# Optimization experiments

Measured on AMD Instinct MI355X. Metric: run time of the kernel, lower is better.

## Reference

```python
import jax, jax.numpy as jnp
import numpy as np

N_NODES = 100000
N_EDGES = 3200000
EMB = 64
K = 2
NUM_GRAPHS = 512


def setup_inputs() -> dict:
    key = jax.random.key(0)
    ks = jax.random.split(key, 12)
    x = jax.random.normal(ks[0], (N_NODES, EMB), dtype=jnp.float32)
    edge_index = jax.random.randint(ks[1], (2, N_EDGES), 0, N_NODES, dtype=jnp.int64)
    edge_attr = jax.random.normal(ks[2], (N_EDGES, 1), dtype=jnp.float32)
    batch = jnp.sort(jax.random.randint(ks[3], (N_NODES,), 0, NUM_GRAPHS, dtype=jnp.int64))
    s = 1.0 / np.sqrt(EMB)
    wn1 = jax.random.normal(ks[4], (EMB, EMB), dtype=jnp.float32) * s
    bn1 = jnp.zeros((EMB,), jnp.float32)
    wn2 = jax.random.normal(ks[5], (EMB, 1), dtype=jnp.float32) * s
    bn2 = jnp.zeros((1,), jnp.float32)
    wc1 = jax.random.normal(ks[6], (EMB, EMB), dtype=jnp.float32) * s
    bc1 = jnp.zeros((EMB,), jnp.float32)
    wc2 = jax.random.normal(ks[7], (EMB, 2 * K * EMB), dtype=jnp.float32) * s
    bc2 = jnp.zeros((2 * K * EMB,), jnp.float32)
    return dict(x=x, edge_index=edge_index, edge_attr=edge_attr, batch=batch,
                wn1=wn1, bn1=bn1, wn2=wn2, bn2=bn2,
                wc1=wc1, bc1=bc1, wc2=wc2, bc2=bc2)


def reference(x, edge_index, edge_attr, batch, wn1, bn1, wn2, bn2, wc1, bc1, wc2, bc2):
    N, C = x.shape
    alpha = 0.1  # APPNP teleport prob
    # --- APPNP(K=1): gcn_norm with self-loops, one propagation step ---
    loops = jnp.arange(N, dtype=edge_index.dtype)
    src = jnp.concatenate([edge_index[0], loops])
    dst = jnp.concatenate([edge_index[1], loops])
    ones = jnp.ones(src.shape[0], dtype=x.dtype)
    deg = jax.ops.segment_sum(ones, dst, num_segments=N)
    dinv = jnp.where(deg > 0, jax.lax.rsqrt(deg), 0.0)
    norm = dinv[src] * dinv[dst]  # [E+N]
    agg = jax.ops.segment_sum(x[src] * norm[:, None], dst, num_segments=N)
    diffuse_x = (1.0 - alpha) * agg + alpha * x  # [N, C]
    # --- node-wise gate: MLP -> global softmax over all nodes ---
    h = jax.nn.relu(diffuse_x @ wn1 + bn1)
    gamma = h @ wn2 + bn2  # [N, 1]
    gamma = jax.nn.softmax(gamma, axis=0)
    # --- per-graph mean pool + channel-wise MLP ---
    sums = jax.ops.segment_sum(diffuse_x, batch, num_segments=NUM_GRAPHS)
    cnt = jax.ops.segment_sum(jnp.ones((N,), x.dtype), batch, num_segments=NUM_GRAPHS)
    pooled = jnp.where(cnt[:, None] > 0, sums / jnp.maximum(cnt, 1.0)[:, None], 0.0)
    pc = jnp.tanh(jax.nn.relu(pooled @ wc1 + bc1) @ wc2 + bc2)  # [B, 2*K*C]
    alpha_kc = pc[:, : K * C].reshape(NUM_GRAPHS, K, C)
    beta_kc = alpha_kc  # faithful to original bug: beta_kc = alpha_kc.reshape(...)
    # --- per-node affine via kron(alpha_kc, gamma_dense) gathered back to nodes ---
    # alpha_batch[b, n, k, c] = alpha_kc[b, k, c] * gamma_dense[b, n]; mask-gather == index by batch
    g = gamma[:, :, None]  # [N, 1, 1]
    a_node = alpha_kc[batch] * g  # [N, K, C]
    b_node = beta_kc[batch] * g  # [N, K, C]
    out = jnp.max(a_node * x[:, None, :] + b_node, axis=1)  # [N, C]
    return out
```

## Files before the change

### kernel.cpp

```cpp
#include <hip/hip_runtime.h>
#include <cstdint>

#define N_NODES   100000
#define N_EDGES   3200000
#define EMB       64
#define NUM_GRAPHS 512
#define NB        391
#define CAP       9216
#define PCHUNK    8192
#define PBLOCKS   391

__device__ __forceinline__ float bflo(unsigned u) { return __uint_as_float(u << 16); }
__device__ __forceinline__ float bfhi(unsigned u) { return __uint_as_float(u & 0xFFFF0000u); }
__device__ __forceinline__ unsigned rne_bf16(float f) {
    unsigned b = __float_as_uint(f);
    return (b + 0x7FFFu + ((b >> 16) & 1u)) >> 16;
}

__global__ void cvt_kernel(const float* __restrict__ x, unsigned* __restrict__ xh) {
    int i = blockIdx.x * 256 + threadIdx.x;
    if (i < N_NODES * EMB / 2) {
        float2 f = ((const float2*)x)[i];
        xh[i] = rne_bf16(f.x) | (rne_bf16(f.y) << 16);
    }
}

__global__ void partition_kernel(const int* __restrict__ ei, int* __restrict__ bcnt,
                                 unsigned* __restrict__ gpairs) {
    __shared__ unsigned sp[PCHUNK];
    __shared__ int scnt[512];
    __shared__ int soff[512];
    __shared__ int scur[512];
    __shared__ int gbase[512];
    __shared__ int s[256];
    int t = threadIdx.x;
    for (int i = t; i < 512; i += 256) scnt[i] = 0;
    __syncthreads();
    int base = blockIdx.x * PCHUNK;
    int lim  = min(N_EDGES - base, PCHUNK);
    for (int k = t; k < lim; k += 256) {
        int d = ei[N_EDGES + base + k];
        atomicAdd(&scnt[d >> 8], 1);
    }
    __syncthreads();
    int a0 = scnt[2 * t], a1 = scnt[2 * t + 1];
    int p = a0 + a1;
    s[t] = p; __syncthreads();
    for (int d = 1; d < 256; d <<= 1) {
        int add = (t >= d) ? s[t - d] : 0;
        __syncthreads();
        s[t] += add;
        __syncthreads();
    }
    int excl = s[t] - p;
    soff[2 * t] = excl;       soff[2 * t + 1] = excl + a0;
    scur[2 * t] = excl;       scur[2 * t + 1] = excl + a0;
    __syncthreads();
    for (int i = t; i < NB; i += 256) gbase[i] = i * CAP + atomicAdd(&bcnt[i], scnt[i]);
    __syncthreads();
    for (int k = t; k < lim; k += 256) {
        int sId = ei[base + k];
        int d   = ei[N_EDGES + base + k];
        int pos = atomicAdd(&scur[d >> 8], 1);
        sp[pos] = (unsigned)sId | ((unsigned)(d & 255) << 17);
    }
    __syncthreads();
    for (int i = t; i < lim; i += 256) {
        unsigned pk = sp[i];
        int lo = 0, hi = NB - 1;
        while (lo < hi) { int mid = (lo + hi + 1) >> 1; if (soff[mid] <= i) lo = mid; else hi = mid - 1; }
        gpairs[gbase[lo] + (i - soff[lo])] = pk;
    }
}

__global__ void bucket_scan_kernel(const int* __restrict__ bcnt, int* __restrict__ bbase) {
    __shared__ int s[512];
    int t = threadIdx.x;
    int v = (t < NB) ? bcnt[t] : 0;
    s[t] = v; __syncthreads();
    for (int d = 1; d < 512; d <<= 1) {
        int add = (t >= d) ? s[t - d] : 0;
        __syncthreads();
        s[t] += add;
        __syncthreads();
    }
    if (t < NB) bbase[t] = s[t] - v;
}

__global__ void bscatter2_kernel(const unsigned* __restrict__ gpairs, const int* __restrict__ bcnt,
                                 const int* __restrict__ bbase, int* __restrict__ ebuf,
                                 int* __restrict__ indeg, int* __restrict__ rowstart,
                                 float* __restrict__ dinv) {
    int b = blockIdx.x, t = threadIdx.x, nlo = b << 8;
    __shared__ int lcnt[256];
    __shared__ int lcur[256];
    __shared__ int s[256];
    lcnt[t] = 0; __syncthreads();
    int cnt = bcnt[b];
    const unsigned* gp = gpairs + (size_t)b * CAP;
    for (int i = t; i < cnt; i += 256) atomicAdd(&lcnt[(gp[i] >> 17) & 255], 1);
    __syncthreads();
    int v = lcnt[t];
    s[t] = v; __syncthreads();
    for (int d = 1; d < 256; d <<= 1) {
        int add = (t >= d) ? s[t - d] : 0;
        __syncthreads();
        s[t] += add;
        __syncthreads();
    }
    int excl = s[t] - v;
    int base = bbase[b];
    int n = nlo + t;
    if (n < N_NODES) {
        indeg[n] = v;
        rowstart[n] = base + excl;
        dinv[n] = rsqrtf((float)(v + 1));
    }
    lcur[t] = base + excl;
    __syncthreads();
    for (int i = t; i < cnt; i += 256) {
        unsigned pk = gp[i];
        int pos = atomicAdd(&lcur[(pk >> 17) & 255], 1);
        ebuf[pos] = (int)(pk & 0x1FFFFu);
    }
}

__global__ void gather_mlp_bf16(const int* __restrict__ ebuf, const int* __restrict__ rowstart,
                                const int* __restrict__ indeg, const float* __restrict__ dinv,
                                const float* __restrict__ x, const unsigned* __restrict__ xh,
                                float* __restrict__ dx,
                                const float* __restrict__ wn1, const float* __restrict__ bn1,
                                const float* __restrict__ wn2, const float* __restrict__ bn2,
                                float* __restrict__ gl) {
    __shared__ float wn1s[EMB * EMB];
    __shared__ float bn1s[EMB];
    __shared__ float wn2s[EMB];
    for (int i = threadIdx.x; i < EMB * EMB; i += blockDim.x) wn1s[i] = wn1[i];
    if (threadIdx.x < EMB) { bn1s[threadIdx.x] = bn1[threadIdx.x]; wn2s[threadIdx.x] = wn2[threadIdx.x]; }
    __syncthreads();

    int wid = (blockIdx.x * blockDim.x + threadIdx.x) >> 6;
    if (wid >= N_NODES) return;
    int n = __builtin_amdgcn_readfirstlane(wid);
    int l = threadIdx.x & 63;
    int g = l >> 3;
    int q = l & 7;
    int start = rowstart[n];
    int cnt   = indeg[n];
    float dn  = dinv[n];
    const uint4* __restrict__ xr = (const uint4*)xh;

    float a0 = 0.f, a1 = 0.f, a2 = 0.f, a3 = 0.f, a4 = 0.f, a5 = 0.f, a6 = 0.f, a7 = 0.f;
    int j = 0;
    for (; j + 16 <= cnt; j += 16) {
        int sA = ebuf[start + j + g];
        int sB = ebuf[start + j + 8 + g];
        float wA = dinv[sA] * dn;
        float wB = dinv[sB] * dn;
        uint4 vA = xr[sA * 8 + q];
        uint4 vB = xr[sB * 8 + q];
        a0 += bflo(vA.x) * wA + bflo(vB.x) * wB;
        a1 += bfhi(vA.x) * wA + bfhi(vB.x) * wB;
        a2 += bflo(vA.y) * wA + bflo(vB.y) * wB;
        a3 += bfhi(vA.y) * wA + bfhi(vB.y) * wB;
        a4 += bflo(vA.z) * wA + bflo(vB.z) * wB;
        a5 += bfhi(vA.z) * wA + bfhi(vB.z) * wB;
        a6 += bflo(vA.w) * wA + bflo(vB.w) * wB;
        a7 += bfhi(vA.w) * wA + bfhi(vB.w) * wB;
    }
    if (j + 8 <= cnt) {
        int sA = ebuf[start + j + g];
        float wA = dinv[sA] * dn;
        uint4 vA = xr[sA * 8 + q];
        a0 += bflo(vA.x) * wA; a1 += bfhi(vA.x) * wA;
        a2 += bflo(vA.y) * wA; a3 += bfhi(vA.y) * wA;
        a4 += bflo(vA.z) * wA; a5 += bfhi(vA.z) * wA;
        a6 += bflo(vA.w) * wA; a7 += bfhi(vA.w) * wA;
        j += 8;
    }
    if (g < cnt - j) {
        int sA = ebuf[start + j + g];
        float wA = dinv[sA] * dn;
        uint4 vA = xr[sA * 8 + q];
        a0 += bflo(vA.x) * wA; a1 += bfhi(vA.x) * wA;
        a2 += bflo(vA.y) * wA; a3 += bfhi(vA.y) * wA;
        a4 += bflo(vA.z) * wA; a5 += bfhi(vA.z) * wA;
        a6 += bflo(vA.w) * wA; a7 += bfhi(vA.w) * wA;
    }
    a0 += __shfl_xor(a0, 8); a0 += __shfl_xor(a0, 16); a0 += __shfl_xor(a0, 32);
    a1 += __shfl_xor(a1, 8); a1 += __shfl_xor(a1, 16); a1 += __shfl_xor(a1, 32);
    a2 += __shfl_xor(a2, 8); a2 += __shfl_xor(a2, 16); a2 += __shfl_xor(a2, 32);
    a3 += __shfl_xor(a3, 8); a3 += __shfl_xor(a3, 16); a3 += __shfl_xor(a3, 32);
    a4 += __shfl_xor(a4, 8); a4 += __shfl_xor(a4, 16); a4 += __shfl_xor(a4, 32);
    a5 += __shfl_xor(a5, 8); a5 += __shfl_xor(a5, 16); a5 += __shfl_xor(a5, 32);
    a6 += __shfl_xor(a6, 8); a6 += __shfl_xor(a6, 16); a6 += __shfl_xor(a6, 32);
    a7 += __shfl_xor(a7, 8); a7 += __shfl_xor(a7, 16); a7 += __shfl_xor(a7, 32);

    const float4* __restrict__ x4 = (const float4*)x;
    float4 xv0 = x4[n * 16 + 2 * q];
    float4 xv1 = x4[n * 16 + 2 * q + 1];
    float s2 = dn * dn;
    float r0 = 0.9f * (a0 + xv0.x * s2) + 0.1f * xv0.x;
    float r1 = 0.9f * (a1 + xv0.y * s2) + 0.1f * xv0.y;
    float r2 = 0.9f * (a2 + xv0.z * s2) + 0.1f * xv0.z;
    float r3 = 0.9f * (a3 + xv0.w * s2) + 0.1f * xv0.w;
    float r4 = 0.9f * (a4 + xv1.x * s2) + 0.1f * xv1.x;
    float r5 = 0.9f * (a5 + xv1.y * s2) + 0.1f * xv1.y;
    float r6 = 0.9f * (a6 + xv1.z * s2) + 0.1f * xv1.z;
    float r7 = 0.9f * (a7 + xv1.w * s2) + 0.1f * xv1.w;
    if (l < 8) {
        float4 w0; w0.x = r0; w0.y = r1; w0.z = r2; w0.w = r3;
        float4 w1; w1.x = r4; w1.y = r5; w1.z = r6; w1.w = r7;
        ((float4*)dx)[n * 16 + 2 * l]     = w0;
        ((float4*)dx)[n * 16 + 2 * l + 1] = w1;
    }

    float rr[8] = {r0, r1, r2, r3, r4, r5, r6, r7};
    float am = bn1s[l];
#pragma unroll
    for (int c = 0; c < EMB; ++c) {
        float b = __shfl(rr[c & 7], c >> 3);
        am += b * wn1s[c * EMB + l];
    }
    float h = fmaxf(am, 0.0f);
    float t = h * wn2s[l];
#pragma unroll
    for (int off = 32; off; off >>= 1) t += __shfl_xor(t, off);
    if (l == 0) gl[n] = t + bn2[0];
}

__global__ void gather_mlp_kernel(const int* __restrict__ ebuf, const int* __restrict__ rowstart,
                                  const int* __restrict__ indeg, const float* __restrict__ dinv,
                                  const float* __restrict__ x, float* __restrict__ dx,
                                  const float* __restrict__ wn1, const float* __restrict__ bn1,
                                  const float* __restrict__ wn2, const float* __restrict__ bn2,
                                  float* __restrict__ gl) {
    __shared__ float wn1s[EMB * EMB];
    __shared__ float bn1s[EMB];
    __shared__ float wn2s[EMB];
    for (int i = threadIdx.x; i < EMB * EMB; i += blockDim.x) wn1s[i] = wn1[i];
    if (threadIdx.x < EMB) { bn1s[threadIdx.x] = bn1[threadIdx.x]; wn2s[threadIdx.x] = wn2[threadIdx.x]; }
    __syncthreads();

    int wid = (blockIdx.x * blockDim.x + threadIdx.x) >> 6;
    if (wid >= N_NODES) return;
    int n = __builtin_amdgcn_readfirstlane(wid);
    int l = threadIdx.x & 63;
    int g = l >> 4;
    int q = l & 15;
    int start = rowstart[n];
    int cnt   = indeg[n];
    float dn  = dinv[n];
    const float4* __restrict__ x4 = (const float4*)x;

    float ax = 0.f, ay = 0.f, az = 0.f, aw = 0.f;
    int j = 0;
    for (; j + 8 <= cnt; j += 8) {
        int sA = ebuf[start + j + g];
        int sB = ebuf[start + j + 4 + g];
        float wA = dinv[sA] * dn;
        float wB = dinv[sB] * dn;
        float4 vA = x4[sA * 16 + q];
        float4 vB = x4[sB * 16 + q];
        ax += vA.x * wA + vB.x * wB;
        ay += vA.y * wA + vB.y * wB;
        az += vA.z * wA + vB.z * wB;
        aw += vA.w * wA + vB.w * wB;
    }
    if (j + 4 <= cnt) {
        int sA = ebuf[start + j + g];
        float wA = dinv[sA] * dn;
        float4 vA = x4[sA * 16 + q];
        ax += vA.x * wA; ay += vA.y * wA; az += vA.z * wA; aw += vA.w * wA;
        j += 4;
    }
    int rem = cnt - j;
    if (g < rem) {
        int sA = ebuf[start + j + g];
        float wA = dinv[sA] * dn;
        float4 vA = x4[sA * 16 + q];
        ax += vA.x * wA; ay += vA.y * wA; az += vA.z * wA; aw += vA.w * wA;
    }
    ax += __shfl_xor(ax, 16); ax += __shfl_xor(ax, 32);
    ay += __shfl_xor(ay, 16); ay += __shfl_xor(ay, 32);
    az += __shfl_xor(az, 16); az += __shfl_xor(az, 32);
    aw += __shfl_xor(aw, 16); aw += __shfl_xor(aw, 32);

    float4 xv = x4[n * 16 + q];
    float s2 = dn * dn;
    float r0 = 0.9f * (ax + xv.x * s2) + 0.1f * xv.x;
    float r1 = 0.9f * (ay + xv.y * s2) + 0.1f * xv.y;
    float r2 = 0.9f * (az + xv.z * s2) + 0.1f * xv.z;
    float r3 = 0.9f * (aw + xv.w * s2) + 0.1f * xv.w;
    if (l < 16) {
        float4 rv; rv.x = r0; rv.y = r1; rv.z = r2; rv.w = r3;
        ((float4*)dx)[n * 16 + q] = rv;
    }
    float rr[4] = {r0, r1, r2, r3};
    float am = bn1s[l];
#pragma unroll
    for (int c = 0; c < EMB; ++c) {
        float b = __shfl(rr[c & 3], c >> 2);
        am += b * wn1s[c * EMB + l];
    }
    float h = fmaxf(am, 0.0f);
    float t = h * wn2s[l];
#pragma unroll
    for (int off = 32; off; off >>= 1) t += __shfl_xor(t, off);
    if (l == 0) gl[n] = t + bn2[0];
}

__global__ void expsum_kernel(const float* __restrict__ gl, float* __restrict__ gsum) {
    __shared__ float red[256];
    float s = 0.0f;
    for (int i = blockIdx.x * blockDim.x + threadIdx.x; i < N_NODES; i += gridDim.x * blockDim.x)
        s += expf(gl[i]);
    red[threadIdx.x] = s; __syncthreads();
    for (int t = 128; t; t >>= 1) {
        if ((int)threadIdx.x < t) red[threadIdx.x] += red[threadIdx.x + t];
        __syncthreads();
    }
    if (threadIdx.x == 0) atomicAdd(gsum, red[0]);
}

__device__ inline int lower_bound_i(const int* a, int n, int key) {
    int lo = 0, hi = n;
    while (lo < hi) {
        int mid = (lo + hi) >> 1;
        if (a[mid] < key) lo = mid + 1; else hi = mid;
    }
    return lo;
}
__global__ void pool_kernel(const float* __restrict__ dx, const int* __restrict__ batch,
                            float* __restrict__ pooled) {
    int g = blockIdx.x;
    int lo = lower_bound_i(batch, N_NODES, g);
    int hi = lower_bound_i(batch, N_NODES, g + 1);
    int lane = threadIdx.x & 63;
    int w = threadIdx.x >> 6;
    float acc = 0.0f;
    for (int n = lo + w; n < hi; n += 4) acc += dx[n * EMB + lane];
    __shared__ float red[4][EMB];
    red[w][lane] = acc; __syncthreads();
    if (threadIdx.x < EMB) {
        float s = red[0][threadIdx.x] + red[1][threadIdx.x] + red[2][threadIdx.x] + red[3][threadIdx.x];
        int cnt = hi - lo;
        pooled[g * EMB + threadIdx.x] = cnt > 0 ? s / (float)cnt : 0.0f;
    }
}

__global__ void graph_mlp_kernel(const float* __restrict__ pooled,
                                 const float* __restrict__ wc1, const float* __restrict__ bc1,
                                 const float* __restrict__ wc2, const float* __restrict__ bc2,
                                 float* __restrict__ alphag) {
    int g = blockIdx.x;
    __shared__ float p[EMB];
    __shared__ float h[EMB];
    if (threadIdx.x < EMB) p[threadIdx.x] = pooled[g * EMB + threadIdx.x];
    __syncthreads();
    if (threadIdx.x < EMB) {
        int j = threadIdx.x;
        float a = bc1[j];
        for (int c = 0; c < EMB; ++c) a += p[c] * wc1[c * EMB + j];
        h[j] = fmaxf(a, 0.0f);
    }
    __syncthreads();
    int o = threadIdx.x;
    float a = bc2[o];
    for (int j = 0; j < EMB; ++j) a += h[j] * wc2[j * 256 + o];
    alphag[g * 128 + o] = tanhf(a);
}

__global__ void final_kernel(const float* __restrict__ x, const int* __restrict__ batch,
                             const float* __restrict__ gl, const float* __restrict__ gsum,
                             const float* __restrict__ alphag, float* __restrict__ out) {
    int n = (blockIdx.x * blockDim.x + threadIdx.x) >> 6;
    if (n >= N_NODES) return;
    int lane = threadIdx.x & 63;
    int g = batch[n];
    float gamma = expf(gl[n]) / gsum[0];
    float a0 = alphag[g * 128 + lane];
    float a1 = alphag[g * 128 + 64 + lane];
    float t = gamma * (x[n * EMB + lane] + 1.0f);
    out[n * EMB + lane] = fmaxf(a0 * t, a1 * t);
}

extern "C" void kernel_launch(void* const* d_in, const int* in_sizes, int n_in,
                              void* d_out, int out_size, void* d_ws, size_t ws_size,
                              hipStream_t stream) {
    const float* x     = (const float*)d_in[0];
    const int*   ei    = (const int*)d_in[1];
    const int*   batch = (const int*)d_in[3];
    const float* wn1 = (const float*)d_in[4];
    const float* bn1 = (const float*)d_in[5];
    const float* wn2 = (const float*)d_in[6];
    const float* bn2 = (const float*)d_in[7];
    const float* wc1 = (const float*)d_in[8];
    const float* bc1 = (const float*)d_in[9];
    const float* wc2 = (const float*)d_in[10];
    const float* bc2 = (const float*)d_in[11];
    float* out = (float*)d_out;

    char* wsb = (char*)d_ws;
    float* dx     = (float*)wsb;
    float* gl     = dx + (size_t)N_NODES * EMB;
    float* dinv   = gl + N_NODES;
    float* pooled = dinv + N_NODES;
    float* alphag = pooled + NUM_GRAPHS * EMB;
    int*   bcnt   = (int*)(alphag + NUM_GRAPHS * 128);
    float* gsum   = (float*)(bcnt + 512);
    int*   bbase  = (int*)(gsum + 1);
    int*   indeg  = bbase + 512;
    int*   rowstart = indeg + N_NODES;
    int*   ebuf   = rowstart + N_NODES;
    unsigned* xh  = (unsigned*)(ebuf + N_EDGES);
    unsigned* gpairs = (unsigned*)dx;

    size_t need_bf16 = (size_t)((char*)(xh + (size_t)N_NODES * EMB / 2) - wsb);
    int use_bf16 = (ws_size >= need_bf16);

    hipMemsetAsync(bcnt, 0, 513 * sizeof(int), stream);
    if (use_bf16)
        cvt_kernel<<<(N_NODES * EMB / 2 + 255) / 256, 256, 0, stream>>>(x, xh);
    partition_kernel<<<PBLOCKS, 256, 0, stream>>>(ei, bcnt, gpairs);
    bucket_scan_kernel<<<1, 512, 0, stream>>>(bcnt, bbase);
    bscatter2_kernel<<<NB, 256, 0, stream>>>(gpairs, bcnt, bbase, ebuf, indeg, rowstart, dinv);
    if (use_bf16)
        gather_mlp_bf16<<<(N_NODES * 64) / 256, 256, 0, stream>>>(ebuf, rowstart, indeg, dinv, x, xh, dx,
                                                                  wn1, bn1, wn2, bn2, gl);
    else
        gather_mlp_kernel<<<(N_NODES * 64) / 256, 256, 0, stream>>>(ebuf, rowstart, indeg, dinv, x, dx,
                                                                    wn1, bn1, wn2, bn2, gl);
    expsum_kernel<<<256, 256, 0, stream>>>(gl, gsum);
    pool_kernel<<<NUM_GRAPHS, 256, 0, stream>>>(dx, batch, pooled);
    graph_mlp_kernel<<<NUM_GRAPHS, 128, 0, stream>>>(pooled, wc1, bc1, wc2, bc2, alphag);
    final_kernel<<<N_NODES / 4, 256, 0, stream>>>(x, batch, gl, gsum, alphag, out);
}
```

Before: 314.8 us.

## Shrink partition chunks, store bucket ids, unroll gather by 32, fuse pool+MLP

Partition chunk size is halved, so more blocks run. Each staged edge now keeps its bucket id in a shared array, which replaces the binary search per edge in the scatter loop. The gather loop is unrolled to four edge groups per iteration so more loads are in flight. The pool and graph-MLP kernels are merged into one launch, which removes the intermediate pooled buffer. In exchange it uses more registers in the gather kernel and more shared memory per partition block, and the extra blocks add more global atomics.

```diff
diff --git a/kernel.cpp b/kernel.cpp
--- a/kernel.cpp
+++ b/kernel.cpp
@@ -7,8 +7,8 @@
 #define NUM_GRAPHS 512
 #define NB        391
 #define CAP       9216
-#define PCHUNK    8192
-#define PBLOCKS   391
+#define PCHUNK    4096
+#define PBLOCKS   ((N_EDGES + PCHUNK - 1) / PCHUNK)
 
 __device__ __forceinline__ float bflo(unsigned u) { return __uint_as_float(u << 16); }
 __device__ __forceinline__ float bfhi(unsigned u) { return __uint_as_float(u & 0xFFFF0000u); }
@@ -28,6 +28,7 @@
 __global__ void partition_kernel(const int* __restrict__ ei, int* __restrict__ bcnt,
                                  unsigned* __restrict__ gpairs) {
     __shared__ unsigned sp[PCHUNK];
+    __shared__ unsigned short sb[PCHUNK];
     __shared__ int scnt[512];
     __shared__ int soff[512];
     __shared__ int scur[512];
@@ -61,15 +62,15 @@
     for (int k = t; k < lim; k += 256) {
         int sId = ei[base + k];
         int d   = ei[N_EDGES + base + k];
-        int pos = atomicAdd(&scur[d >> 8], 1);
+        int b   = d >> 8;
+        int pos = atomicAdd(&scur[b], 1);
         sp[pos] = (unsigned)sId | ((unsigned)(d & 255) << 17);
+        sb[pos] = (unsigned short)b;
     }
     __syncthreads();
     for (int i = t; i < lim; i += 256) {
-        unsigned pk = sp[i];
-        int lo = 0, hi = NB - 1;
-        while (lo < hi) { int mid = (lo + hi + 1) >> 1; if (soff[mid] <= i) lo = mid; else hi = mid - 1; }
-        gpairs[gbase[lo] + (i - soff[lo])] = pk;
+        int b = sb[i];
+        gpairs[gbase[b] + (i - soff[b])] = sp[i];
     }
 }
 
@@ -152,7 +153,29 @@
 
     float a0 = 0.f, a1 = 0.f, a2 = 0.f, a3 = 0.f, a4 = 0.f, a5 = 0.f, a6 = 0.f, a7 = 0.f;
     int j = 0;
-    for (; j + 16 <= cnt; j += 16) {
+    for (; j + 32 <= cnt; j += 32) {
+        int sA = ebuf[start + j + g];
+        int sB = ebuf[start + j + 8 + g];
+        int sC = ebuf[start + j + 16 + g];
+        int sD = ebuf[start + j + 24 + g];
+        float wA = dinv[sA] * dn;
+        float wB = dinv[sB] * dn;
+        float wC = dinv[sC] * dn;
+        float wD = dinv[sD] * dn;
+        uint4 vA = xr[sA * 8 + q];
+        uint4 vB = xr[sB * 8 + q];
+        uint4 vC = xr[sC * 8 + q];
+        uint4 vD = xr[sD * 8 + q];
+        a0 += bflo(vA.x) * wA + bflo(vB.x) * wB + bflo(vC.x) * wC + bflo(vD.x) * wD;
+        a1 += bfhi(vA.x) * wA + bfhi(vB.x) * wB + bfhi(vC.x) * wC + bfhi(vD.x) * wD;
+        a2 += bflo(vA.y) * wA + bflo(vB.y) * wB + bflo(vC.y) * wC + bflo(vD.y) * wD;
+        a3 += bfhi(vA.y) * wA + bfhi(vB.y) * wB + bfhi(vC.y) * wC + bfhi(vD.y) * wD;
+        a4 += bflo(vA.z) * wA + bflo(vB.z) * wB + bflo(vC.z) * wC + bflo(vD.z) * wD;
+        a5 += bfhi(vA.z) * wA + bfhi(vB.z) * wB + bfhi(vC.z) * wC + bfhi(vD.z) * wD;
+        a6 += bflo(vA.w) * wA + bflo(vB.w) * wB + bflo(vC.w) * wC + bflo(vD.w) * wD;
+        a7 += bfhi(vA.w) * wA + bfhi(vB.w) * wB + bfhi(vC.w) * wC + bfhi(vD.w) * wD;
+    }
+    if (j + 16 <= cnt) {
         int sA = ebuf[start + j + g];
         int sB = ebuf[start + j + 8 + g];
         float wA = dinv[sA] * dn;
@@ -167,6 +190,7 @@
         a5 += bfhi(vA.z) * wA + bfhi(vB.z) * wB;
         a6 += bflo(vA.w) * wA + bflo(vB.w) * wB;
         a7 += bfhi(vA.w) * wA + bfhi(vB.w) * wB;
+        j += 16;
     }
     if (j + 8 <= cnt) {
         int sA = ebuf[start + j + g];
@@ -331,8 +355,10 @@
     }
     return lo;
 }
-__global__ void pool_kernel(const float* __restrict__ dx, const int* __restrict__ batch,
-                            float* __restrict__ pooled) {
+__global__ void poolmlp_kernel(const float* __restrict__ dx, const int* __restrict__ batch,
+                               const float* __restrict__ wc1, const float* __restrict__ bc1,
+                               const float* __restrict__ wc2, const float* __restrict__ bc2,
+                               float* __restrict__ alphag) {
     int g = blockIdx.x;
     int lo = lower_bound_i(batch, N_NODES, g);
     int hi = lower_bound_i(batch, N_NODES, g + 1);
@@ -341,22 +367,14 @@
     float acc = 0.0f;
     for (int n = lo + w; n < hi; n += 4) acc += dx[n * EMB + lane];
     __shared__ float red[4][EMB];
+    __shared__ float p[EMB];
+    __shared__ float h[EMB];
     red[w][lane] = acc; __syncthreads();
     if (threadIdx.x < EMB) {
         float s = red[0][threadIdx.x] + red[1][threadIdx.x] + red[2][threadIdx.x] + red[3][threadIdx.x];
         int cnt = hi - lo;
-        pooled[g * EMB + threadIdx.x] = cnt > 0 ? s / (float)cnt : 0.0f;
-    }
-}
-
-__global__ void graph_mlp_kernel(const float* __restrict__ pooled,
-                                 const float* __restrict__ wc1, const float* __restrict__ bc1,
-                                 const float* __restrict__ wc2, const float* __restrict__ bc2,
-                                 float* __restrict__ alphag) {
-    int g = blockIdx.x;
-    __shared__ float p[EMB];
-    __shared__ float h[EMB];
-    if (threadIdx.x < EMB) p[threadIdx.x] = pooled[g * EMB + threadIdx.x];
+        p[threadIdx.x] = cnt > 0 ? s / (float)cnt : 0.0f;
+    }
     __syncthreads();
     if (threadIdx.x < EMB) {
         int j = threadIdx.x;
@@ -365,10 +383,12 @@
         h[j] = fmaxf(a, 0.0f);
     }
     __syncthreads();
-    int o = threadIdx.x;
-    float a = bc2[o];
-    for (int j = 0; j < EMB; ++j) a += h[j] * wc2[j * 256 + o];
-    alphag[g * 128 + o] = tanhf(a);
+    if (threadIdx.x < 128) {
+        int o = threadIdx.x;
+        float a = bc2[o];
+        for (int j = 0; j < EMB; ++j) a += h[j] * wc2[j * 256 + o];
+        alphag[g * 128 + o] = tanhf(a);
+    }
 }
 
 __global__ void final_kernel(const float* __restrict__ x, const int* __restrict__ batch,
@@ -432,7 +452,6 @@
         gather_mlp_kernel<<<(N_NODES * 64) / 256, 256, 0, stream>>>(ebuf, rowstart, indeg, dinv, x, dx,
                                                                     wn1, bn1, wn2, bn2, gl);
     expsum_kernel<<<256, 256, 0, stream>>>(gl, gsum);
-    pool_kernel<<<NUM_GRAPHS, 256, 0, stream>>>(dx, batch, pooled);
-    graph_mlp_kernel<<<NUM_GRAPHS, 128, 0, stream>>>(pooled, wc1, bc1, wc2, bc2, alphag);
+    poolmlp_kernel<<<NUM_GRAPHS, 256, 0, stream>>>(dx, batch, wc1, bc1, wc2, bc2, alphag);
     final_kernel<<<N_NODES / 4, 256, 0, stream>>>(x, batch, gl, gsum, alphag, out);
 }
```

Result: faster. 295.8 us (-6.0%).
